# Kernel optimization log

Hardware: AMD Instinct MI355X
Metric: run time of the kernel (lower is better)

The kernel has to match this reference:

```python
import jax, jax.numpy as jnp
import numpy as np

DIM = 1024
NUM_HEADS = 16
HEAD_DIM = DIM // NUM_HEADS
SCALE = HEAD_DIM ** -0.5
CAUSAL = True


def setup_inputs() -> dict:
    key = jax.random.key(0)
    k_x, k_qkv, k_proj, k_pb = jax.random.split(key, 4)
    B, S = 4, 2048
    x = jax.random.normal(k_x, (B, S, DIM), dtype=jnp.float32)
    # nn.Linear(dim, 3*dim, bias=False): weight [3*dim, dim]; store transposed [dim, 3*dim]
    w_qkv = jax.random.normal(k_qkv, (DIM, 3 * DIM), dtype=jnp.float32) * (DIM ** -0.5)
    w_proj = jax.random.normal(k_proj, (DIM, DIM), dtype=jnp.float32) * (DIM ** -0.5)
    b_proj = jax.random.normal(k_pb, (DIM,), dtype=jnp.float32) * 0.01
    return {"x": x, "w_qkv": w_qkv, "w_proj": w_proj, "b_proj": b_proj}


def reference(x, w_qkv, w_proj, b_proj):
    B, S, C = x.shape
    # qkv: [B, S, 3, H, D] -> q,k,v each [B, H, S, D]
    qkv = (x @ w_qkv).reshape(B, S, 3, NUM_HEADS, HEAD_DIM)
    qkv = jnp.transpose(qkv, (2, 0, 3, 1, 4))
    q, k, v = qkv[0], qkv[1], qkv[2]
    # scores [B, H, S, S]
    attn = jnp.einsum('bhqd,bhkd->bhqk', q, k) * SCALE
    if CAUSAL:
        causal_mask = jnp.triu(jnp.ones((S, S), dtype=bool), k=1)
        attn = jnp.where(causal_mask, -jnp.inf, attn)
    attn = jax.nn.softmax(attn, axis=-1)
    out = jnp.einsum('bhqk,bhkd->bhqd', attn, v)
    out = jnp.transpose(out, (0, 2, 1, 3)).reshape(B, S, C)
    return out @ w_proj + b_proj
```

## Files before the change

### kernel.cpp

```cpp
#include <hip/hip_runtime.h>
#include <hip/hip_bf16.h>
#include <math.h>

#define DIMC 1024
#define NHEADS 16
#define HDIM 64
#define BATCH 4
#define SEQ 2048
#define NROWS (BATCH * SEQ)
#define ATTN_SCALE 0.125f
#define LOG2E 1.4426950408889634f

typedef __attribute__((ext_vector_type(8))) short short8;
typedef __attribute__((ext_vector_type(4))) short short4v;
typedef __attribute__((ext_vector_type(4))) float f32x4;

static __device__ __forceinline__ short f2bf(float f) {
    __hip_bfloat16 h = __float2bfloat16(f);
    return *reinterpret_cast<short*>(&h);
}

__global__ __launch_bounds__(256)
void xcvt(const float* __restrict__ in, unsigned short* __restrict__ out) {
    int i = blockIdx.x * 256 + threadIdx.x;
    const float4* p = reinterpret_cast<const float4*>(in) + 2 * i;
    float4 a = p[0], b = p[1];
    short8 pk;
    pk[0] = f2bf(a.x); pk[1] = f2bf(a.y); pk[2] = f2bf(a.z); pk[3] = f2bf(a.w);
    pk[4] = f2bf(b.x); pk[5] = f2bf(b.y); pk[6] = f2bf(b.z); pk[7] = f2bf(b.w);
    reinterpret_cast<short8*>(out)[i] = pk;
}

__global__ __launch_bounds__(256)
void transpose_cvt(const float* __restrict__ src, unsigned short* __restrict__ dst,
                   int N) {
    __shared__ float t[64][65];
    const int tid = threadIdx.x;
    const int cb = blockIdx.x * 64;
    const int rb = blockIdx.y * 64;
#pragma unroll
    for (int e = 0; e < 4; e++) {
        int idx = tid + e * 256;
        int row = idx >> 4;
        int c4 = (idx & 15) << 2;
        *reinterpret_cast<float4*>(&t[row][c4]) =
            *reinterpret_cast<const float4*>(&src[(size_t)(rb + row) * N + cb + c4]);
    }
    __syncthreads();
#pragma unroll
    for (int e = 0; e < 2; e++) {
        int idx = tid + e * 256;
        int col = idx >> 3;
        int k8 = (idx & 7) << 3;
        short8 pk;
#pragma unroll
        for (int j = 0; j < 8; j++) pk[j] = f2bf(t[k8 + j][col]);
        *reinterpret_cast<short8*>(&dst[(size_t)(cb + col) * 1024 + rb + k8]) = pk;
    }
}

__global__ __launch_bounds__(256)
void qkv_gemm_mfma(const unsigned short* __restrict__ Xbf,
                   const unsigned short* __restrict__ Wt,
                   unsigned short* __restrict__ qo, unsigned short* __restrict__ ko,
                   unsigned short* __restrict__ vt) {
    __shared__ short Alds[4][128][8];
    __shared__ short Blds[4][128][8];
    const int tid = threadIdx.x;
    const int lane = tid & 63;
    const int wave = tid >> 6;
    const int wr = wave >> 1, wc = wave & 1;
    const int rowbase = blockIdx.y * 128;
    const int colbase = blockIdx.x * 128;
    const int kb = lane >> 4, li = lane & 15, g = lane >> 4;

    f32x4 acc[4][4];
#pragma unroll
    for (int m = 0; m < 4; m++)
#pragma unroll
        for (int n = 0; n < 4; n++) acc[m][n] = (f32x4){0.f, 0.f, 0.f, 0.f};

    for (int k0 = 0; k0 < DIMC; k0 += 32) {
#pragma unroll
        for (int e = 0; e < 2; e++) {
            int idx = tid + e * 256;
            int akb = idx & 3, row = idx >> 2;
            *reinterpret_cast<short8*>(&Alds[akb][row][0]) =
                *reinterpret_cast<const short8*>(
                    &Xbf[(size_t)(rowbase + row) * DIMC + k0 + akb * 8]);
            *reinterpret_cast<short8*>(&Blds[akb][row][0]) =
                *reinterpret_cast<const short8*>(
                    &Wt[(size_t)(colbase + row) * 1024 + k0 + akb * 8]);
        }
        __syncthreads();
        short8 af[4], bfr[4];
#pragma unroll
        for (int m = 0; m < 4; m++)
            af[m] = *reinterpret_cast<const short8*>(
                &Alds[kb][wr * 64 + m * 16 + li][0]);
#pragma unroll
        for (int n = 0; n < 4; n++)
            bfr[n] = *reinterpret_cast<const short8*>(
                &Blds[kb][wc * 64 + n * 16 + li][0]);
#pragma unroll
        for (int m = 0; m < 4; m++)
#pragma unroll
            for (int n = 0; n < 4; n++)
                acc[m][n] = __builtin_amdgcn_mfma_f32_16x16x32_bf16(
                    af[m], bfr[n], acc[m][n], 0, 0, 0);
        __syncthreads();
    }

    const int col0 = colbase + wc * 64;
    const int three = col0 >> 10;
    const int h = (col0 & 1023) >> 6;
    if (three < 2) {
        unsigned short* dst = (three == 0) ? qo : ko;
        const float mult = (three == 0) ? (ATTN_SCALE * LOG2E) : 1.0f;
#pragma unroll
        for (int n = 0; n < 4; n++) {
            int d = n * 16 + li;
#pragma unroll
            for (int m = 0; m < 4; m++) {
                int r0 = rowbase + wr * 64 + m * 16 + g * 4;
                int b = r0 >> 11;
                size_t base = ((size_t)(b * NHEADS + h) * SEQ) * HDIM + d;
#pragma unroll
                for (int r = 0; r < 4; r++) {
                    int s = (r0 + r) & 2047;
                    dst[base + (size_t)s * HDIM] = (unsigned short)f2bf(acc[m][n][r] * mult);
                }
            }
        }
    } else {
#pragma unroll
        for (int n = 0; n < 4; n++) {
            int d = n * 16 + li;
#pragma unroll
            for (int m = 0; m < 4; m++) {
                int r0 = rowbase + wr * 64 + m * 16 + g * 4;
                int b = r0 >> 11, s0 = r0 & 2047;
                short4v pk;
#pragma unroll
                for (int r = 0; r < 4; r++) pk[r] = f2bf(acc[m][n][r]);
                *reinterpret_cast<short4v*>(
                    &vt[((size_t)(b * NHEADS + h) * HDIM + d) * SEQ + s0]) = pk;
            }
        }
    }
}

__global__ __launch_bounds__(256)
void proj_gemm_mfma(const unsigned short* __restrict__ Abf,
                    const unsigned short* __restrict__ Wt,
                    const float* __restrict__ bias, float* __restrict__ out) {
    __shared__ short Alds[4][128][8];
    __shared__ short Blds[4][128][8];
    const int tid = threadIdx.x;
    const int lane = tid & 63;
    const int wave = tid >> 6;
    const int wr = wave >> 1, wc = wave & 1;
    const int rowbase = blockIdx.y * 128;
    const int colbase = blockIdx.x * 128;
    const int kb = lane >> 4, li = lane & 15;

    f32x4 acc[4][4];
#pragma unroll
    for (int m = 0; m < 4; m++)
#pragma unroll
        for (int n = 0; n < 4; n++) acc[m][n] = (f32x4){0.f, 0.f, 0.f, 0.f};

    for (int k0 = 0; k0 < DIMC; k0 += 32) {
#pragma unroll
        for (int e = 0; e < 2; e++) {
            int idx = tid + e * 256;
            int akb = idx & 3, row = idx >> 2;
            *reinterpret_cast<short8*>(&Alds[akb][row][0]) =
                *reinterpret_cast<const short8*>(
                    &Abf[(size_t)(rowbase + row) * DIMC + k0 + akb * 8]);
            *reinterpret_cast<short8*>(&Blds[akb][row][0]) =
                *reinterpret_cast<const short8*>(
                    &Wt[(size_t)(colbase + row) * 1024 + k0 + akb * 8]);
        }
        __syncthreads();
        short8 af[4], bfr[4];
#pragma unroll
        for (int m = 0; m < 4; m++)
            af[m] = *reinterpret_cast<const short8*>(
                &Alds[kb][wr * 64 + m * 16 + li][0]);
#pragma unroll
        for (int n = 0; n < 4; n++)
            bfr[n] = *reinterpret_cast<const short8*>(
                &Blds[kb][wc * 64 + n * 16 + li][0]);
#pragma unroll
        for (int m = 0; m < 4; m++)
#pragma unroll
            for (int n = 0; n < 4; n++)
                acc[m][n] = __builtin_amdgcn_mfma_f32_16x16x32_bf16(
                    af[m], bfr[n], acc[m][n], 0, 0, 0);
        __syncthreads();
    }

#pragma unroll
    for (int n = 0; n < 4; n++) {
        int col = colbase + wc * 64 + n * 16 + li;
        float bv = bias[col];
#pragma unroll
        for (int m = 0; m < 4; m++) {
            int r0 = rowbase + wr * 64 + m * 16 + (lane >> 4) * 4;
#pragma unroll
            for (int r = 0; r < 4; r++)
                out[(size_t)(r0 + r) * DIMC + col] = acc[m][n][r] + bv;
        }
    }
}

__global__ __launch_bounds__(256)
void flash_attn_mfma(const unsigned short* __restrict__ qg,
                     const unsigned short* __restrict__ kg,
                     const unsigned short* __restrict__ vt,
                     unsigned short* __restrict__ og) {
    __shared__ short Klds[2][64][64];
    __shared__ short Vlds[2][64][64];
    __shared__ short Plds[4][32][64];
    const int tid = threadIdx.x;
    const int lane = tid & 63;
    const int w = tid >> 6;
    const int g = lane >> 4, li = lane & 15;
    const int sw = li & 7;
    const int bh = blockIdx.y;
    const size_t head = (size_t)bh * SEQ * HDIM;
    const int b = bh >> 4, h = bh & 15;

    const int c0r = tid >> 3, c0c = tid & 7;
    const int c1r = (tid + 256) >> 3, c1c = tid & 7;

    for (int pass = 0; pass < 2; pass++) {
        const int qtile = pass ? (15 - (int)blockIdx.x) : (int)blockIdx.x;
        const int qbase = qtile * 128;
        const int qw = qbase + w * 32;
        const int nt = 2 * qtile + 2;

        short8 bq[2][2];
#pragma unroll
        for (int n = 0; n < 2; n++)
#pragma unroll
            for (int ds = 0; ds < 2; ds++)
                bq[n][ds] = *reinterpret_cast<const short8*>(
                    &qg[head + (size_t)(qw + li + 16 * n) * HDIM + ds * 32 + g * 8]);

        f32x4 accO[4][2];
#pragma unroll
        for (int df = 0; df < 4; df++)
#pragma unroll
            for (int n = 0; n < 2; n++) accO[df][n] = (f32x4){0.f, 0.f, 0.f, 0.f};
        float mrow[2] = {-INFINITY, -INFINITY};
        float lrow[2] = {0.f, 0.f};

        short8 kreg0, kreg1, vreg0, vreg1;
        kreg0 = *reinterpret_cast<const short8*>(&kg[head + (size_t)c0r * HDIM + c0c * 8]);
        vreg0 = *reinterpret_cast<const short8*>(&vt[head + (size_t)c0r * SEQ + c0c * 8]);
        kreg1 = *reinterpret_cast<const short8*>(&kg[head + (size_t)c1r * HDIM + c1c * 8]);
        vreg1 = *reinterpret_cast<const short8*>(&vt[head + (size_t)c1r * SEQ + c1c * 8]);
        *reinterpret_cast<short8*>(&Klds[0][c0r][(c0c ^ (c0r & 7)) * 8]) = kreg0;
        *reinterpret_cast<short8*>(&Vlds[0][c0r][(c0c ^ (c0r & 7)) * 8]) = vreg0;
        *reinterpret_cast<short8*>(&Klds[0][c1r][(c1c ^ (c1r & 7)) * 8]) = kreg1;
        *reinterpret_cast<short8*>(&Vlds[0][c1r][(c1c ^ (c1r & 7)) * 8]) = vreg1;
        __syncthreads();

        for (int t = 0; t < nt; t++) {
            const int kvbase = t * 64;
            const int buf = t & 1;
            const bool more = (t + 1 < nt);
            if (more) {
                const int kb2 = kvbase + 64;
                kreg0 = *reinterpret_cast<const short8*>(
                    &kg[head + (size_t)(kb2 + c0r) * HDIM + c0c * 8]);
                vreg0 = *reinterpret_cast<const short8*>(
                    &vt[head + (size_t)c0r * SEQ + kb2 + c0c * 8]);
                kreg1 = *reinterpret_cast<const short8*>(
                    &kg[head + (size_t)(kb2 + c1r) * HDIM + c1c * 8]);
                vreg1 = *reinterpret_cast<const short8*>(
                    &vt[head + (size_t)c1r * SEQ + kb2 + c1c * 8]);
            }

            if (kvbase <= qw + 31) {
                f32x4 s[4][2];
#pragma unroll
                for (int m = 0; m < 4; m++)
#pragma unroll
                    for (int n = 0; n < 2; n++) s[m][n] = (f32x4){0.f, 0.f, 0.f, 0.f};
#pragma unroll
                for (int ds = 0; ds < 2; ds++) {
                    short8 ak[4];
#pragma unroll
                    for (int m = 0; m < 4; m++)
                        ak[m] = *reinterpret_cast<const short8*>(
                            &Klds[buf][li + 16 * m][(((ds * 4 + g) ^ sw)) * 8]);
#pragma unroll
                    for (int m = 0; m < 4; m++)
#pragma unroll
                        for (int n = 0; n < 2; n++)
                            s[m][n] = __builtin_amdgcn_mfma_f32_16x16x32_bf16(
                                ak[m], bq[n][ds], s[m][n], 0, 0, 0);
                }
                const bool diag = (kvbase + 63 > qw);
                float tmax[2] = {-INFINITY, -INFINITY};
#pragma unroll
                for (int n = 0; n < 2; n++) {
                    int q = qw + li + 16 * n;
#pragma unroll
                    for (int m = 0; m < 4; m++) {
#pragma unroll
                        for (int r = 0; r < 4; r++) {
                            if (diag) {
                                int kv = kvbase + 16 * m + 4 * g + r;
                                if (kv > q) s[m][n][r] = -INFINITY;
                            }
                            tmax[n] = fmaxf(tmax[n], s[m][n][r]);
                        }
                    }
                }
                float corr[2];
#pragma unroll
                for (int n = 0; n < 2; n++) {
                    tmax[n] = fmaxf(tmax[n], __shfl_xor(tmax[n], 16));
                    tmax[n] = fmaxf(tmax[n], __shfl_xor(tmax[n], 32));
                    float mnew = fmaxf(mrow[n], tmax[n]);
                    corr[n] = __builtin_amdgcn_exp2f(mrow[n] - mnew);
                    mrow[n] = mnew;
                }
                float tsum[2] = {0.f, 0.f};
#pragma unroll
                for (int m = 0; m < 4; m++) {
#pragma unroll
                    for (int n = 0; n < 2; n++) {
                        float p0 = __builtin_amdgcn_exp2f(s[m][n][0] - mrow[n]);
                        float p1 = __builtin_amdgcn_exp2f(s[m][n][1] - mrow[n]);
                        float p2 = __builtin_amdgcn_exp2f(s[m][n][2] - mrow[n]);
                        float p3 = __builtin_amdgcn_exp2f(s[m][n][3] - mrow[n]);
                        tsum[n] += (p0 + p1) + (p2 + p3);
                        short4v pk;
                        pk[0] = f2bf(p0); pk[1] = f2bf(p1);
                        pk[2] = f2bf(p2); pk[3] = f2bf(p3);
                        *reinterpret_cast<short4v*>(
                            &Plds[w][li + 16 * n]
                                 [((2 * m + (g >> 1)) ^ sw) * 8 + (g & 1) * 4]) = pk;
                    }
                }
#pragma unroll
                for (int n = 0; n < 2; n++) {
                    tsum[n] += __shfl_xor(tsum[n], 16);
                    tsum[n] += __shfl_xor(tsum[n], 32);
                    lrow[n] = lrow[n] * corr[n] + tsum[n];
                }
                bool nore = (corr[0] == 1.0f) && (corr[1] == 1.0f);
                if (!__all((int)nore)) {
#pragma unroll
                    for (int df = 0; df < 4; df++)
#pragma unroll
                        for (int n = 0; n < 2; n++) {
                            accO[df][n][0] *= corr[n]; accO[df][n][1] *= corr[n];
                            accO[df][n][2] *= corr[n]; accO[df][n][3] *= corr[n];
                        }
                }
#pragma unroll
                for (int ks = 0; ks < 2; ks++) {
                    short8 av[4], bp[2];
#pragma unroll
                    for (int df = 0; df < 4; df++)
                        av[df] = *reinterpret_cast<const short8*>(
                            &Vlds[buf][li + 16 * df][((ks * 4 + g) ^ sw) * 8]);
#pragma unroll
                    for (int n = 0; n < 2; n++)
                        bp[n] = *reinterpret_cast<const short8*>(
                            &Plds[w][li + 16 * n][((ks * 4 + g) ^ sw) * 8]);
#pragma unroll
                    for (int df = 0; df < 4; df++)
#pragma unroll
                        for (int n = 0; n < 2; n++)
                            accO[df][n] = __builtin_amdgcn_mfma_f32_16x16x32_bf16(
                                av[df], bp[n], accO[df][n], 0, 0, 0);
                }
            }

            if (more) {
                const int nbuf = buf ^ 1;
                *reinterpret_cast<short8*>(&Klds[nbuf][c0r][(c0c ^ (c0r & 7)) * 8]) = kreg0;
                *reinterpret_cast<short8*>(&Vlds[nbuf][c0r][(c0c ^ (c0r & 7)) * 8]) = vreg0;
                *reinterpret_cast<short8*>(&Klds[nbuf][c1r][(c1c ^ (c1r & 7)) * 8]) = kreg1;
                *reinterpret_cast<short8*>(&Vlds[nbuf][c1r][(c1c ^ (c1r & 7)) * 8]) = vreg1;
            }
            __syncthreads();
        }

#pragma unroll
        for (int n = 0; n < 2; n++) {
            float inv = 1.0f / lrow[n];
            int q = qw + li + 16 * n;
            size_t rowoff = (size_t)(b * SEQ + q) * DIMC + h * HDIM;
#pragma unroll
            for (int df = 0; df < 4; df++) {
                short4v pk;
#pragma unroll
                for (int r = 0; r < 4; r++) pk[r] = f2bf(accO[df][n][r] * inv);
                *reinterpret_cast<short4v*>(&og[rowoff + 16 * df + 4 * g]) = pk;
            }
        }
        __syncthreads();
    }
}

extern "C" void kernel_launch(void* const* d_in, const int* in_sizes, int n_in,
                              void* d_out, int out_size, void* d_ws, size_t ws_size,
                              hipStream_t stream) {
    const float* x      = (const float*)d_in[0];
    const float* w_qkv  = (const float*)d_in[1];
    const float* w_proj = (const float*)d_in[2];
    const float* b_proj = (const float*)d_in[3];
    float* out = (float*)d_out;

    char* w = (char*)d_ws;
    unsigned short* qb  = (unsigned short*)(w);
    unsigned short* kb  = (unsigned short*)(w + ((size_t)16 << 20));
    unsigned short* vtb = (unsigned short*)(w + ((size_t)32 << 20));
    unsigned short* ao  = (unsigned short*)(w + ((size_t)48 << 20));
    unsigned short* wqt = (unsigned short*)(w + ((size_t)64 << 20));
    unsigned short* wpt = (unsigned short*)(w + ((size_t)72 << 20));
    unsigned short* xbf = (unsigned short*)(w + ((size_t)80 << 20));

    xcvt<<<NROWS * DIMC / (256 * 8), 256, 0, stream>>>(x, xbf);
    transpose_cvt<<<dim3(3 * DIMC / 64, DIMC / 64), 256, 0, stream>>>(w_qkv, wqt, 3 * DIMC);
    transpose_cvt<<<dim3(DIMC / 64, DIMC / 64), 256, 0, stream>>>(w_proj, wpt, DIMC);
    qkv_gemm_mfma<<<dim3(3 * DIMC / 128, NROWS / 128), 256, 0, stream>>>(xbf, wqt, qb, kb, vtb);
    flash_attn_mfma<<<dim3(SEQ / 256, BATCH * NHEADS), 256, 0, stream>>>(qb, kb, vtb, ao);
    proj_gemm_mfma<<<dim3(DIMC / 128, NROWS / 128), 256, 0, stream>>>(ao, wpt, b_proj, out);
}
```

Measured before the change: 306.9 us.

## Load GEMM tiles directly into LDS and swizzle attention block order

Both MFMA GEMMs now stage A and B tiles with global_load_lds DMA into a row-major [128][32] LDS layout. This skips the register round-trip of the old vector loads followed by LDS stores. The flash attention launch becomes a 1D grid whose block index is remapped, so consecutive blocks map to different heads and spread across XCDs/L2. The new LDS layout may introduce bank conflicts on fragment reads, and the DMA path is used with no extra waitcnt beyond __syncthreads.

```diff
diff --git a/kernel.cpp b/kernel.cpp
--- a/kernel.cpp
+++ b/kernel.cpp
@@ -18,6 +18,12 @@
 static __device__ __forceinline__ short f2bf(float f) {
     __hip_bfloat16 h = __float2bfloat16(f);
     return *reinterpret_cast<short*>(&h);
+}
+
+static __device__ __forceinline__ void gload16(const void* g, void* l) {
+    __builtin_amdgcn_global_load_lds(
+        (const __attribute__((address_space(1))) unsigned int*)g,
+        (__attribute__((address_space(3))) unsigned int*)l, 16, 0, 0);
 }
 
 __global__ __launch_bounds__(256)
@@ -64,15 +70,20 @@
                    const unsigned short* __restrict__ Wt,
                    unsigned short* __restrict__ qo, unsigned short* __restrict__ ko,
                    unsigned short* __restrict__ vt) {
-    __shared__ short Alds[4][128][8];
-    __shared__ short Blds[4][128][8];
+    __shared__ short Alds[128][32];
+    __shared__ short Blds[128][32];
     const int tid = threadIdx.x;
     const int lane = tid & 63;
     const int wave = tid >> 6;
     const int wr = wave >> 1, wc = wave & 1;
     const int rowbase = blockIdx.y * 128;
     const int colbase = blockIdx.x * 128;
-    const int kb = lane >> 4, li = lane & 15, g = lane >> 4;
+    const int g = lane >> 4, li = lane & 15;
+    const int srow0 = (wave * 2 + 0) * 16 + (lane >> 2);
+    const int srow1 = (wave * 2 + 1) * 16 + (lane >> 2);
+    const int scol = (lane & 3) * 8;
+    short* aflat = &Alds[0][0];
+    short* bflat = &Blds[0][0];
 
     f32x4 acc[4][4];
 #pragma unroll
@@ -81,27 +92,22 @@
         for (int n = 0; n < 4; n++) acc[m][n] = (f32x4){0.f, 0.f, 0.f, 0.f};
 
     for (int k0 = 0; k0 < DIMC; k0 += 32) {
-#pragma unroll
-        for (int e = 0; e < 2; e++) {
-            int idx = tid + e * 256;
-            int akb = idx & 3, row = idx >> 2;
-            *reinterpret_cast<short8*>(&Alds[akb][row][0]) =
-                *reinterpret_cast<const short8*>(
-                    &Xbf[(size_t)(rowbase + row) * DIMC + k0 + akb * 8]);
-            *reinterpret_cast<short8*>(&Blds[akb][row][0]) =
-                *reinterpret_cast<const short8*>(
-                    &Wt[(size_t)(colbase + row) * 1024 + k0 + akb * 8]);
-        }
+        gload16(&Xbf[(size_t)(rowbase + srow0) * DIMC + k0 + scol],
+                aflat + (wave * 2 + 0) * 512);
+        gload16(&Xbf[(size_t)(rowbase + srow1) * DIMC + k0 + scol],
+                aflat + (wave * 2 + 1) * 512);
+        gload16(&Wt[(size_t)(colbase + srow0) * 1024 + k0 + scol],
+                bflat + (wave * 2 + 0) * 512);
+        gload16(&Wt[(size_t)(colbase + srow1) * 1024 + k0 + scol],
+                bflat + (wave * 2 + 1) * 512);
         __syncthreads();
         short8 af[4], bfr[4];
 #pragma unroll
         for (int m = 0; m < 4; m++)
-            af[m] = *reinterpret_cast<const short8*>(
-                &Alds[kb][wr * 64 + m * 16 + li][0]);
+            af[m] = *reinterpret_cast<const short8*>(&Alds[wr * 64 + m * 16 + li][g * 8]);
 #pragma unroll
         for (int n = 0; n < 4; n++)
-            bfr[n] = *reinterpret_cast<const short8*>(
-                &Blds[kb][wc * 64 + n * 16 + li][0]);
+            bfr[n] = *reinterpret_cast<const short8*>(&Blds[wc * 64 + n * 16 + li][g * 8]);
 #pragma unroll
         for (int m = 0; m < 4; m++)
 #pragma unroll
@@ -154,15 +160,20 @@
 void proj_gemm_mfma(const unsigned short* __restrict__ Abf,
                     const unsigned short* __restrict__ Wt,
                     const float* __restrict__ bias, float* __restrict__ out) {
-    __shared__ short Alds[4][128][8];
-    __shared__ short Blds[4][128][8];
+    __shared__ short Alds[128][32];
+    __shared__ short Blds[128][32];
     const int tid = threadIdx.x;
     const int lane = tid & 63;
     const int wave = tid >> 6;
     const int wr = wave >> 1, wc = wave & 1;
     const int rowbase = blockIdx.y * 128;
     const int colbase = blockIdx.x * 128;
-    const int kb = lane >> 4, li = lane & 15;
+    const int g = lane >> 4, li = lane & 15;
+    const int srow0 = (wave * 2 + 0) * 16 + (lane >> 2);
+    const int srow1 = (wave * 2 + 1) * 16 + (lane >> 2);
+    const int scol = (lane & 3) * 8;
+    short* aflat = &Alds[0][0];
+    short* bflat = &Blds[0][0];
 
     f32x4 acc[4][4];
 #pragma unroll
@@ -171,27 +182,22 @@
         for (int n = 0; n < 4; n++) acc[m][n] = (f32x4){0.f, 0.f, 0.f, 0.f};
 
     for (int k0 = 0; k0 < DIMC; k0 += 32) {
-#pragma unroll
-        for (int e = 0; e < 2; e++) {
-            int idx = tid + e * 256;
-            int akb = idx & 3, row = idx >> 2;
-            *reinterpret_cast<short8*>(&Alds[akb][row][0]) =
-                *reinterpret_cast<const short8*>(
-                    &Abf[(size_t)(rowbase + row) * DIMC + k0 + akb * 8]);
-            *reinterpret_cast<short8*>(&Blds[akb][row][0]) =
-                *reinterpret_cast<const short8*>(
-                    &Wt[(size_t)(colbase + row) * 1024 + k0 + akb * 8]);
-        }
+        gload16(&Abf[(size_t)(rowbase + srow0) * DIMC + k0 + scol],
+                aflat + (wave * 2 + 0) * 512);
+        gload16(&Abf[(size_t)(rowbase + srow1) * DIMC + k0 + scol],
+                aflat + (wave * 2 + 1) * 512);
+        gload16(&Wt[(size_t)(colbase + srow0) * 1024 + k0 + scol],
+                bflat + (wave * 2 + 0) * 512);
+        gload16(&Wt[(size_t)(colbase + srow1) * 1024 + k0 + scol],
+                bflat + (wave * 2 + 1) * 512);
         __syncthreads();
         short8 af[4], bfr[4];
 #pragma unroll
         for (int m = 0; m < 4; m++)
-            af[m] = *reinterpret_cast<const short8*>(
-                &Alds[kb][wr * 64 + m * 16 + li][0]);
+            af[m] = *reinterpret_cast<const short8*>(&Alds[wr * 64 + m * 16 + li][g * 8]);
 #pragma unroll
         for (int n = 0; n < 4; n++)
-            bfr[n] = *reinterpret_cast<const short8*>(
-                &Blds[kb][wc * 64 + n * 16 + li][0]);
+            bfr[n] = *reinterpret_cast<const short8*>(&Blds[wc * 64 + n * 16 + li][g * 8]);
 #pragma unroll
         for (int m = 0; m < 4; m++)
 #pragma unroll
@@ -207,7 +213,7 @@
         float bv = bias[col];
 #pragma unroll
         for (int m = 0; m < 4; m++) {
-            int r0 = rowbase + wr * 64 + m * 16 + (lane >> 4) * 4;
+            int r0 = rowbase + wr * 64 + m * 16 + g * 4;
 #pragma unroll
             for (int r = 0; r < 4; r++)
                 out[(size_t)(r0 + r) * DIMC + col] = acc[m][n][r] + bv;
@@ -228,7 +234,10 @@
     const int w = tid >> 6;
     const int g = lane >> 4, li = lane & 15;
     const int sw = li & 7;
-    const int bh = blockIdx.y;
+    const int orig = blockIdx.x;
+    const int swz = (orig & 7) * 64 + (orig >> 3);
+    const int bx = swz & 7;
+    const int bh = swz >> 3;
     const size_t head = (size_t)bh * SEQ * HDIM;
     const int b = bh >> 4, h = bh & 15;
 
@@ -236,7 +245,7 @@
     const int c1r = (tid + 256) >> 3, c1c = tid & 7;
 
     for (int pass = 0; pass < 2; pass++) {
-        const int qtile = pass ? (15 - (int)blockIdx.x) : (int)blockIdx.x;
+        const int qtile = pass ? (15 - bx) : bx;
         const int qbase = qtile * 128;
         const int qw = qbase + w * 32;
         const int nt = 2 * qtile + 2;
@@ -433,6 +442,6 @@
     transpose_cvt<<<dim3(3 * DIMC / 64, DIMC / 64), 256, 0, stream>>>(w_qkv, wqt, 3 * DIMC);
     transpose_cvt<<<dim3(DIMC / 64, DIMC / 64), 256, 0, stream>>>(w_proj, wpt, DIMC);
     qkv_gemm_mfma<<<dim3(3 * DIMC / 128, NROWS / 128), 256, 0, stream>>>(xbf, wqt, qb, kb, vtb);
-    flash_attn_mfma<<<dim3(SEQ / 256, BATCH * NHEADS), 256, 0, stream>>>(qb, kb, vtb, ao);
+    flash_attn_mfma<<<512, 256, 0, stream>>>(qb, kb, vtb, ao);
     proj_gemm_mfma<<<dim3(DIMC / 128, NROWS / 128), 256, 0, stream>>>(ao, wpt, b_proj, out);
 }
```

After: 272.0 us. -11.4%, faster.
